# Performance work log

Measured on AMD Instinct MI355X. Metric: run time of the kernel, lower is better.

Reference implementation:

```python
import jax, jax.numpy as jnp
import numpy as np

DIM = 512
N_HEADS = 8
HEAD_DIM = DIM // N_HEADS
TOP_K_RATIO = 0.25
B, L = 2, 2048


def setup_inputs() -> dict:
    key = jax.random.key(0)
    k1, k2, k3, k4, k5 = jax.random.split(key, 5)
    s = 0.02
    return {
        "x": jax.random.normal(k1, (B, L, DIM), jnp.float32),
        "w_qkv": jax.random.normal(k2, (3 * DIM, DIM), jnp.float32) * s,
        "b_qkv": jnp.zeros((3 * DIM,), jnp.float32),
        "w_out": jax.random.normal(k3, (DIM, DIM), jnp.float32) * s,
        "b_out": jnp.zeros((DIM,), jnp.float32),
    }


def reference(x, w_qkv, b_qkv, w_out, b_out):
    Bx, Lx, C = x.shape
    scale = HEAD_DIM ** -0.5
    top_k = max(1, int(TOP_K_RATIO * Lx))

    qkv = x @ w_qkv.T + b_qkv  # [B, L, 3*C]
    qkv = qkv.reshape(Bx, Lx, 3, N_HEADS, HEAD_DIM)
    q, k, v = qkv[:, :, 0], qkv[:, :, 1], qkv[:, :, 2]  # [B, L, H, D]

    scores = jnp.einsum('blhd,bshd->bhls', q, k) * scale  # [B, H, L, L]

    _, top_idx = jax.lax.top_k(scores, top_k)  # [B, H, L, K]
    bi = jnp.arange(Bx)[:, None, None, None]
    hi = jnp.arange(N_HEADS)[None, :, None, None]
    li = jnp.arange(Lx)[None, None, :, None]
    mask = jnp.zeros(scores.shape, bool).at[bi, hi, li, top_idx].set(True)

    masked = jnp.where(mask, scores, -jnp.inf)
    probs = jax.nn.softmax(masked, axis=-1)  # [B, H, L, L]

    out = jnp.einsum('bhls,bshd->blhd', probs, v).reshape(Bx, Lx, C)
    return out @ w_out.T + b_out
```

## Files before the change

kernel.cpp:

```cpp
#include <hip/hip_runtime.h>

#define B_ 2
#define L_ 2048
#define DIM_ 512
#define NH_ 8
#define HD_ 64
#define TOPK_ 512

typedef __attribute__((ext_vector_type(8))) short short8;
typedef __attribute__((ext_vector_type(4))) float f32x4;
typedef unsigned short ushort_t;

__device__ __forceinline__ unsigned f2ord(float f) {
  unsigned u = __float_as_uint(f);
  return (u >> 31) ? ~u : (u | 0x80000000u);
}
__device__ __forceinline__ float ord2f(unsigned k) {
  unsigned u = (k >> 31) ? (k ^ 0x80000000u) : ~k;
  return __uint_as_float(u);
}
__device__ __forceinline__ ushort_t bfrne(float f) {
  unsigned u = __float_as_uint(f);
  return (ushort_t)((u + 0x7FFFu + ((u >> 16) & 1u)) >> 16);
}

__global__ __launch_bounds__(256) void split_k(
    const float* __restrict__ src, ushort_t* __restrict__ dh,
    ushort_t* __restrict__ dl, int n8)
{
  const int i = blockIdx.x * 256 + threadIdx.x;
  if (i >= n8) return;
  const float4 a = ((const float4*)src)[2 * i];
  const float4 b = ((const float4*)src)[2 * i + 1];
  float f[8] = {a.x, a.y, a.z, a.w, b.x, b.y, b.z, b.w};
  short8 h, l;
#pragma unroll
  for (int j = 0; j < 8; ++j) {
    const ushort_t hi = bfrne(f[j]);
    const float hf = __uint_as_float((unsigned)hi << 16);
    h[j] = (short)hi;
    l[j] = (short)bfrne(f[j] - hf);
  }
  *(short8*)(dh + 8 * (size_t)i) = h;
  *(short8*)(dl + 8 * (size_t)i) = l;
}

template<int EPI>
__global__ __launch_bounds__(128, 2) void mgemm(
    const ushort_t* __restrict__ Ah, const ushort_t* __restrict__ Al,
    const ushort_t* __restrict__ Bh, const ushort_t* __restrict__ Bl,
    const float* __restrict__ bias, int N, float* __restrict__ out,
    ushort_t* __restrict__ Qh, ushort_t* __restrict__ Ql,
    ushort_t* __restrict__ Kh, ushort_t* __restrict__ Kl,
    ushort_t* __restrict__ Vt)
{
  constexpr int K = DIM_;
  const int lane = threadIdx.x & 63, wid = threadIdx.x >> 6;
  const int m0 = blockIdx.y * 64;
  const int n0 = blockIdx.x * 64 + wid * 32;
  const int arow = lane & 15, agrp = lane >> 4;

  f32x4 acc[4][2];
#pragma unroll
  for (int rt = 0; rt < 4; ++rt)
#pragma unroll
    for (int ct = 0; ct < 2; ++ct) acc[rt][ct] = (f32x4){0.f, 0.f, 0.f, 0.f};

#pragma unroll 4
  for (int ks = 0; ks < K / 32; ++ks) {
    const int ko = ks * 32 + agrp * 8;
    short8 ah[4], al[4];
#pragma unroll
    for (int rt = 0; rt < 4; ++rt) {
      const size_t ao = (size_t)(m0 + rt * 16 + arow) * K + ko;
      ah[rt] = *(const short8*)(Ah + ao);
      al[rt] = *(const short8*)(Al + ao);
    }
    short8 bhf[2], blf[2];
#pragma unroll
    for (int ct = 0; ct < 2; ++ct) {
      const size_t bo = (size_t)(n0 + ct * 16 + arow) * K + ko;
      bhf[ct] = *(const short8*)(Bh + bo);
      blf[ct] = *(const short8*)(Bl + bo);
    }
#pragma unroll
    for (int rt = 0; rt < 4; ++rt)
#pragma unroll
      for (int ct = 0; ct < 2; ++ct) {
        acc[rt][ct] = __builtin_amdgcn_mfma_f32_16x16x32_bf16(ah[rt], bhf[ct], acc[rt][ct], 0, 0, 0);
        acc[rt][ct] = __builtin_amdgcn_mfma_f32_16x16x32_bf16(al[rt], bhf[ct], acc[rt][ct], 0, 0, 0);
        acc[rt][ct] = __builtin_amdgcn_mfma_f32_16x16x32_bf16(ah[rt], blf[ct], acc[rt][ct], 0, 0, 0);
      }
  }

#pragma unroll
  for (int rt = 0; rt < 4; ++rt) {
#pragma unroll
    for (int ct = 0; ct < 2; ++ct) {
#pragma unroll
      for (int rr = 0; rr < 4; ++rr) {
        const int m = m0 + rt * 16 + agrp * 4 + rr;
        const int n = n0 + ct * 16 + arow;
        float v = acc[rt][ct][rr] + bias[n];
        if (EPI == 0) {
          out[(size_t)m * N + n] = v;
        } else {
          const int b = m >> 11, l = m & (L_ - 1);
          const int which = n >> 9, h = (n >> 6) & (NH_ - 1), d = n & (HD_ - 1);
          const int bh = b * NH_ + h;
          if (which == 0) {
            v *= 0.125f;
            ushort_t hi = bfrne(v);
            float hf = __uint_as_float((unsigned)hi << 16);
            ushort_t lo = bfrne(v - hf);
            const size_t o = ((size_t)bh * L_ + l) * HD_ + d;
            Qh[o] = hi; Ql[o] = lo;
          } else if (which == 1) {
            ushort_t hi = bfrne(v);
            float hf = __uint_as_float((unsigned)hi << 16);
            ushort_t lo = bfrne(v - hf);
            const size_t o = ((size_t)bh * L_ + l) * HD_ + d;
            Kh[o] = hi; Kl[o] = lo;
          } else {
            Vt[((size_t)bh * HD_ + d) * L_ + l] = bfrne(v);
          }
        }
      }
    }
  }
}

__global__ __launch_bounds__(256, 4) void sgemm_k(
    const ushort_t* __restrict__ Qh, const ushort_t* __restrict__ Ql,
    const ushort_t* __restrict__ Kh, const ushort_t* __restrict__ Kl,
    float* __restrict__ S, int row0, int CH)
{
  const int lane = threadIdx.x & 63, wid = threadIdx.x >> 6;
  const int bh = blockIdx.z;
  const int m0 = blockIdx.y * 64;
  const int n0 = blockIdx.x * 128 + wid * 32;
  const int arow = lane & 15, agrp = lane >> 4;

  short8 kh[2][2], kl[2][2];
#pragma unroll
  for (int kt = 0; kt < 2; ++kt) {
    const size_t ka = ((size_t)bh * L_ + n0 + kt * 16 + arow) * HD_ + agrp * 8;
    kh[kt][0] = *(const short8*)(Kh + ka);
    kh[kt][1] = *(const short8*)(Kh + ka + 32);
    kl[kt][0] = *(const short8*)(Kl + ka);
    kl[kt][1] = *(const short8*)(Kl + ka + 32);
  }

  float* schunk = S + (size_t)bh * CH * L_;
#pragma unroll
  for (int rt = 0; rt < 4; ++rt) {
    const size_t qa = ((size_t)bh * L_ + row0 + m0 + rt * 16 + arow) * HD_ + agrp * 8;
    const short8 qh0 = *(const short8*)(Qh + qa);
    const short8 qh1 = *(const short8*)(Qh + qa + 32);
    const short8 ql0 = *(const short8*)(Ql + qa);
    const short8 ql1 = *(const short8*)(Ql + qa + 32);
#pragma unroll
    for (int kt = 0; kt < 2; ++kt) {
      f32x4 aA = {0.f, 0.f, 0.f, 0.f}, aB = {0.f, 0.f, 0.f, 0.f};
      aA = __builtin_amdgcn_mfma_f32_16x16x32_bf16(qh0, kh[kt][0], aA, 0, 0, 0);
      aB = __builtin_amdgcn_mfma_f32_16x16x32_bf16(qh1, kh[kt][1], aB, 0, 0, 0);
      aA = __builtin_amdgcn_mfma_f32_16x16x32_bf16(ql0, kh[kt][0], aA, 0, 0, 0);
      aB = __builtin_amdgcn_mfma_f32_16x16x32_bf16(ql1, kh[kt][1], aB, 0, 0, 0);
      aA = __builtin_amdgcn_mfma_f32_16x16x32_bf16(qh0, kl[kt][0], aA, 0, 0, 0);
      aB = __builtin_amdgcn_mfma_f32_16x16x32_bf16(qh1, kl[kt][1], aB, 0, 0, 0);
#pragma unroll
      for (int rr = 0; rr < 4; ++rr)
        schunk[(size_t)(m0 + rt * 16 + agrp * 4 + rr) * L_ + n0 + kt * 16 + arow]
            = aA[rr] + aB[rr];
    }
  }
}

__global__ __launch_bounds__(512, 8) void selpv_k(
    const float* __restrict__ S, const ushort_t* __restrict__ Vt,
    ushort_t* __restrict__ AOh, ushort_t* __restrict__ AOl, int row0, int CH)
{
  __shared__ ushort_t pl[8][2056];
  __shared__ float invs[8];
  float* red = (float*)&pl[0][0];

  const int tid = threadIdx.x, lane = tid & 63, wid = tid >> 6;
  const int bh = blockIdx.y;
  const int blk = blockIdx.x;
  const int arow = lane & 15, agrp = lane >> 4;

  {
    const float* srow = S + ((size_t)bh * CH + blk * 8 + wid) * L_;
    unsigned keys[32];
    float mx = -3.0e38f;
#pragma unroll
    for (int t = 0; t < 32; ++t) {
      const float s = srow[lane + 64 * t];
      keys[t] = f2ord(s);
      mx = fmaxf(mx, s);
    }
#pragma unroll
    for (int off = 32; off; off >>= 1) mx = fmaxf(mx, __shfl_xor(mx, off));

    unsigned P = 0;
#pragma unroll 1
    for (int bit = 31; bit >= 8; --bit) {
      const unsigned cand = P | (1u << bit);
      int c = 0;
#pragma unroll
      for (int t = 0; t < 32; ++t)
        c += (int)__popcll(__ballot(keys[t] >= cand));
      if (c >= TOPK_) P = cand;
    }

    int base = 0;
    float part = 0.f;
#pragma unroll
    for (int t = 0; t < 32; ++t) {
      const bool sel = keys[t] >= P;
      const unsigned long long mb = __ballot(sel);
      const int pos = base + (int)__popcll(mb & ((1ull << lane) - 1ull));
      const float p = (sel && pos < TOPK_) ? __expf(ord2f(keys[t]) - mx) : 0.f;
      pl[wid][lane + 64 * t] = bfrne(p);
      part += p;
      base += (int)__popcll(mb);
    }
#pragma unroll
    for (int off = 32; off; off >>= 1) part += __shfl_xor(part, off);
    if (lane == 0) invs[wid] = 1.f / part;
  }
  __syncthreads();

  f32x4 o0 = {0.f,0.f,0.f,0.f}, o1 = o0, o2 = o0, o3 = o0;
  {
    const int key00 = wid << 8;
    const size_t vrow = ((size_t)bh * HD_ + arow) * L_;
#pragma unroll 2
    for (int ks = 0; ks < 8; ++ks) {
      const int kb = key00 + ks * 32 + agrp * 8;
      const short8 pa = *(const short8*)&pl[arow & 7][kb];
      const size_t vb0 = vrow + kb;
      const short8 v0 = *(const short8*)(Vt + vb0);
      const short8 v1 = *(const short8*)(Vt + vb0 + 16 * L_);
      const short8 v2 = *(const short8*)(Vt + vb0 + 32 * L_);
      const short8 v3 = *(const short8*)(Vt + vb0 + 48 * L_);
      o0 = __builtin_amdgcn_mfma_f32_16x16x32_bf16(pa, v0, o0, 0, 0, 0);
      o1 = __builtin_amdgcn_mfma_f32_16x16x32_bf16(pa, v1, o1, 0, 0, 0);
      o2 = __builtin_amdgcn_mfma_f32_16x16x32_bf16(pa, v2, o2, 0, 0, 0);
      o3 = __builtin_amdgcn_mfma_f32_16x16x32_bf16(pa, v3, o3, 0, 0, 0);
    }
  }
  __syncthreads();

  if (agrp < 2) {
#pragma unroll
    for (int rr = 0; rr < 4; ++rr) {
      const int row = agrp * 4 + rr;
      red[wid * 512 + row * 64 +  0 + arow] = o0[rr];
      red[wid * 512 + row * 64 + 16 + arow] = o1[rr];
      red[wid * 512 + row * 64 + 32 + arow] = o2[rr];
      red[wid * 512 + row * 64 + 48 + arow] = o3[rr];
    }
  }
  __syncthreads();
  {
    const int b = bh >> 3, h = bh & 7;
    const int r = tid >> 6, d = tid & 63;
    float s = 0.f;
#pragma unroll
    for (int w = 0; w < 8; ++w) s += red[w * 512 + r * 64 + d];
    const float sv = s * invs[r];
    const ushort_t hi = bfrne(sv);
    const float hf = __uint_as_float((unsigned)hi << 16);
    const size_t oidx = ((size_t)(b * L_ + row0 + blk * 8 + r)) * DIM_ + h * HD_ + d;
    AOh[oidx] = hi;
    AOl[oidx] = bfrne(sv - hf);
  }
}

__global__ __launch_bounds__(1024, 1) void attn_fused_k(
    const ushort_t* __restrict__ Qh, const ushort_t* __restrict__ Ql,
    const ushort_t* __restrict__ Kh, const ushort_t* __restrict__ Kl,
    const ushort_t* __restrict__ Vt,
    ushort_t* __restrict__ AOh, ushort_t* __restrict__ AOl)
{
  __shared__ float sc[16][2052];
  __shared__ float invs[16];

  const int tid = threadIdx.x, lane = tid & 63, wid = tid >> 6;
  const int bh = blockIdx.x >> 7;
  const int l0 = (blockIdx.x & 127) << 4;
  const int arow = lane & 15, agrp = lane >> 4;
  const int key00 = wid << 7;

  const size_t qbase = ((size_t)bh * L_ + l0 + arow) * HD_ + agrp * 8;
  const short8 qh0 = *(const short8*)(Qh + qbase);
  const short8 qh1 = *(const short8*)(Qh + qbase + 32);
  const short8 ql0 = *(const short8*)(Ql + qbase);
  const short8 ql1 = *(const short8*)(Ql + qbase + 32);

  {
#pragma unroll
    for (int t = 0; t < 8; ++t) {
      const int key0 = key00 + t * 16;
      const size_t ka = ((size_t)bh * L_ + key0 + arow) * HD_ + agrp * 8;
      const short8 kh0 = *(const short8*)(Kh + ka);
      const short8 kh1 = *(const short8*)(Kh + ka + 32);
      const short8 kl0 = *(const short8*)(Kl + ka);
      const short8 kl1 = *(const short8*)(Kl + ka + 32);
      f32x4 aA = {0.f, 0.f, 0.f, 0.f}, aB = {0.f, 0.f, 0.f, 0.f};
      aA = __builtin_amdgcn_mfma_f32_16x16x32_bf16(qh0, kh0, aA, 0, 0, 0);
      aB = __builtin_amdgcn_mfma_f32_16x16x32_bf16(qh1, kh1, aB, 0, 0, 0);
      aA = __builtin_amdgcn_mfma_f32_16x16x32_bf16(ql0, kh0, aA, 0, 0, 0);
      aB = __builtin_amdgcn_mfma_f32_16x16x32_bf16(ql1, kh1, aB, 0, 0, 0);
      aA = __builtin_amdgcn_mfma_f32_16x16x32_bf16(qh0, kl0, aA, 0, 0, 0);
      aB = __builtin_amdgcn_mfma_f32_16x16x32_bf16(qh1, kl1, aB, 0, 0, 0);
#pragma unroll
      for (int rr = 0; rr < 4; ++rr)
        sc[agrp * 4 + rr][key0 + arow] = aA[rr] + aB[rr];
    }
  }
  __syncthreads();

  {
    const int r = wid;
    unsigned keys[32];
    float mx = -3.0e38f;
#pragma unroll
    for (int t = 0; t < 32; ++t) {
      const float s = sc[r][lane + 64 * t];
      keys[t] = f2ord(s);
      mx = fmaxf(mx, s);
    }
#pragma unroll
    for (int off = 32; off; off >>= 1) mx = fmaxf(mx, __shfl_xor(mx, off));

    unsigned P = 0;
#pragma unroll 1
    for (int bit = 31; bit >= 8; --bit) {
      const unsigned cand = P | (1u << bit);
      int c = 0;
#pragma unroll
      for (int t = 0; t < 32; ++t)
        c += (int)__popcll(__ballot(keys[t] >= cand));
      if (c >= TOPK_) P = cand;
    }

    int base = 0;
    float part = 0.f;
#pragma unroll
    for (int t = 0; t < 32; ++t) {
      const bool sel = keys[t] >= P;
      const unsigned long long mb = __ballot(sel);
      const int pos = base + (int)__popcll(mb & ((1ull << lane) - 1ull));
      const float p = (sel && pos < TOPK_) ? __expf(ord2f(keys[t]) - mx) : 0.f;
      sc[r][lane + 64 * t] = p;
      part += p;
      base += (int)__popcll(mb);
    }
#pragma unroll
    for (int off = 32; off; off >>= 1) part += __shfl_xor(part, off);
    if (lane == 0) invs[r] = 1.f / part;
  }
  __syncthreads();

  f32x4 o0 = {0.f,0.f,0.f,0.f}, o1 = o0, o2 = o0, o3 = o0;
  {
    const size_t vrow = ((size_t)bh * HD_ + arow) * L_;
#pragma unroll
    for (int ks = 0; ks < 4; ++ks) {
      const int kb = key00 + ks * 32 + agrp * 8;
      float pf[8];
      *(float4*)&pf[0] = *(const float4*)&sc[arow][kb];
      *(float4*)&pf[4] = *(const float4*)&sc[arow][kb + 4];
      short8 pa;
#pragma unroll
      for (int j = 0; j < 8; ++j) pa[j] = (short)bfrne(pf[j]);
      const size_t vb0 = vrow + kb;
      const short8 v0 = *(const short8*)(Vt + vb0);
      const short8 v1 = *(const short8*)(Vt + vb0 + 16 * L_);
      const short8 v2 = *(const short8*)(Vt + vb0 + 32 * L_);
      const short8 v3 = *(const short8*)(Vt + vb0 + 48 * L_);
      o0 = __builtin_amdgcn_mfma_f32_16x16x32_bf16(pa, v0, o0, 0, 0, 0);
      o1 = __builtin_amdgcn_mfma_f32_16x16x32_bf16(pa, v1, o1, 0, 0, 0);
      o2 = __builtin_amdgcn_mfma_f32_16x16x32_bf16(pa, v2, o2, 0, 0, 0);
      o3 = __builtin_amdgcn_mfma_f32_16x16x32_bf16(pa, v3, o3, 0, 0, 0);
    }
  }
  __syncthreads();

  float* red = &sc[0][0];
  {
#pragma unroll
    for (int rr = 0; rr < 4; ++rr) {
      const int row = agrp * 4 + rr;
      red[wid * 1024 + row * 64 +  0 + arow] = o0[rr];
      red[wid * 1024 + row * 64 + 16 + arow] = o1[rr];
      red[wid * 1024 + row * 64 + 32 + arow] = o2[rr];
      red[wid * 1024 + row * 64 + 48 + arow] = o3[rr];
    }
  }
  __syncthreads();
  {
    const int b = bh >> 3, h = bh & 7;
    const int r = tid >> 6, d = tid & 63;
    float s = 0.f;
#pragma unroll
    for (int w = 0; w < 16; ++w) s += red[w * 1024 + tid];
    const float sv = s * invs[r];
    const ushort_t hi = bfrne(sv);
    const float hf = __uint_as_float((unsigned)hi << 16);
    const size_t oidx = ((size_t)(b * L_ + l0 + r)) * DIM_ + h * HD_ + d;
    AOh[oidx] = hi;
    AOl[oidx] = bfrne(sv - hf);
  }
}

extern "C" void kernel_launch(void* const* d_in, const int* in_sizes, int n_in,
                              void* d_out, int out_size, void* d_ws, size_t ws_size,
                              hipStream_t stream) {
  const float* x     = (const float*)d_in[0];
  const float* w_qkv = (const float*)d_in[1];
  const float* b_qkv = (const float*)d_in[2];
  const float* w_out = (const float*)d_in[3];
  const float* b_out = (const float*)d_in[4];
  float* out = (float*)d_out;

  const size_t NE  = (size_t)B_ * NH_ * L_ * HD_;
  const size_t NWQ = (size_t)3 * DIM_ * DIM_;
  const size_t NWO = (size_t)DIM_ * DIM_;

  ushort_t* us  = (ushort_t*)d_ws;
  ushort_t* Qh  = us;
  ushort_t* Ql  = Qh + NE;
  ushort_t* Kh  = Ql + NE;
  ushort_t* Kl  = Kh + NE;
  ushort_t* Vt  = Kl + NE;
  ushort_t* AOh = Vt + NE;
  ushort_t* AOl = AOh + NE;
  ushort_t* woh = AOl + NE;
  ushort_t* wol = woh + NWO;
  ushort_t* xh  = wol + NWO;
  ushort_t* xl  = xh + NE;
  ushort_t* wqh = xl + NE;
  ushort_t* wql = wqh + NWQ;
  float*    S   = (float*)xh;

  const size_t sOffB   = (size_t)(7 * NE + 2 * NWO) * sizeof(ushort_t);
  const size_t perRowB = (size_t)B_ * NH_ * L_ * sizeof(float);

  int CH = 0;
  const int cands[6] = {1024, 512, 2048, 256, 128, 64};
  for (int i = 0; i < 6; ++i)
    if (sOffB + (size_t)cands[i] * perRowB <= ws_size) { CH = cands[i]; break; }

  split_k<<<(int)((NE  / 8 + 255) / 256), 256, 0, stream>>>(x,     xh,  xl,  (int)(NE  / 8));
  split_k<<<(int)((NWQ / 8 + 255) / 256), 256, 0, stream>>>(w_qkv, wqh, wql, (int)(NWQ / 8));
  split_k<<<(int)((NWO / 8 + 255) / 256), 256, 0, stream>>>(w_out, woh, wol, (int)(NWO / 8));

  mgemm<1><<<dim3((3 * DIM_) / 64, (B_ * L_) / 64), 128, 0, stream>>>(
      xh, xl, wqh, wql, b_qkv, 3 * DIM_, nullptr, Qh, Ql, Kh, Kl, Vt);

  if (CH) {
    for (int row0 = 0; row0 < L_; row0 += CH) {
      sgemm_k<<<dim3(L_ / 128, CH / 64, B_ * NH_), 256, 0, stream>>>(
          Qh, Ql, Kh, Kl, S, row0, CH);
      selpv_k<<<dim3(CH / 8, B_ * NH_), 512, 0, stream>>>(S, Vt, AOh, AOl, row0, CH);
    }
  } else {
    attn_fused_k<<<dim3(B_ * NH_ * (L_ / 16)), 1024, 0, stream>>>(
        Qh, Ql, Kh, Kl, Vt, AOh, AOl);
  }

  mgemm<0><<<dim3(DIM_ / 64, (B_ * L_) / 64), 128, 0, stream>>>(
      AOh, AOl, woh, wol, b_out, DIM_, out, nullptr, nullptr, nullptr, nullptr, nullptr);
}
```

Baseline: 385.8 us.

## Merge score GEMM and select-PV into one kernel with double-buffered chunks

Replaces the separate score-GEMM and top-k/PV kernels with a single kernel whose blocks are split by index between computing scores for chunk i+1 and doing selection plus PV for chunk i. Two score buffers of 512 rows are used in ping-pong order across five launches, so the memory-heavy GEMM writes overlap the compute-heavy selection within one launch. The GEMM path now runs with 512 threads covering 256 columns per block. The cost is a larger workspace requirement and mixed block types, which can leave resources unbalanced.

```diff
diff --git a/kernel.cpp b/kernel.cpp
--- a/kernel.cpp
+++ b/kernel.cpp
@@ -6,6 +6,7 @@
 #define NH_ 8
 #define HD_ 64
 #define TOPK_ 512
+#define SCH_ 512
 
 typedef __attribute__((ext_vector_type(8))) short short8;
 typedef __attribute__((ext_vector_type(4))) float f32x4;
@@ -130,67 +131,71 @@
   }
 }
 
-__global__ __launch_bounds__(256, 4) void sgemm_k(
+__global__ __launch_bounds__(512, 4) void fat_k(
     const ushort_t* __restrict__ Qh, const ushort_t* __restrict__ Ql,
     const ushort_t* __restrict__ Kh, const ushort_t* __restrict__ Kl,
-    float* __restrict__ S, int row0, int CH)
-{
-  const int lane = threadIdx.x & 63, wid = threadIdx.x >> 6;
-  const int bh = blockIdx.z;
-  const int m0 = blockIdx.y * 64;
-  const int n0 = blockIdx.x * 128 + wid * 32;
-  const int arow = lane & 15, agrp = lane >> 4;
-
-  short8 kh[2][2], kl[2][2];
-#pragma unroll
-  for (int kt = 0; kt < 2; ++kt) {
-    const size_t ka = ((size_t)bh * L_ + n0 + kt * 16 + arow) * HD_ + agrp * 8;
-    kh[kt][0] = *(const short8*)(Kh + ka);
-    kh[kt][1] = *(const short8*)(Kh + ka + 32);
-    kl[kt][0] = *(const short8*)(Kl + ka);
-    kl[kt][1] = *(const short8*)(Kl + ka + 32);
-  }
-
-  float* schunk = S + (size_t)bh * CH * L_;
-#pragma unroll
-  for (int rt = 0; rt < 4; ++rt) {
-    const size_t qa = ((size_t)bh * L_ + row0 + m0 + rt * 16 + arow) * HD_ + agrp * 8;
-    const short8 qh0 = *(const short8*)(Qh + qa);
-    const short8 qh1 = *(const short8*)(Qh + qa + 32);
-    const short8 ql0 = *(const short8*)(Ql + qa);
-    const short8 ql1 = *(const short8*)(Ql + qa + 32);
-#pragma unroll
-    for (int kt = 0; kt < 2; ++kt) {
-      f32x4 aA = {0.f, 0.f, 0.f, 0.f}, aB = {0.f, 0.f, 0.f, 0.f};
-      aA = __builtin_amdgcn_mfma_f32_16x16x32_bf16(qh0, kh[kt][0], aA, 0, 0, 0);
-      aB = __builtin_amdgcn_mfma_f32_16x16x32_bf16(qh1, kh[kt][1], aB, 0, 0, 0);
-      aA = __builtin_amdgcn_mfma_f32_16x16x32_bf16(ql0, kh[kt][0], aA, 0, 0, 0);
-      aB = __builtin_amdgcn_mfma_f32_16x16x32_bf16(ql1, kh[kt][1], aB, 0, 0, 0);
-      aA = __builtin_amdgcn_mfma_f32_16x16x32_bf16(qh0, kl[kt][0], aA, 0, 0, 0);
-      aB = __builtin_amdgcn_mfma_f32_16x16x32_bf16(qh1, kl[kt][1], aB, 0, 0, 0);
-#pragma unroll
-      for (int rr = 0; rr < 4; ++rr)
-        schunk[(size_t)(m0 + rt * 16 + agrp * 4 + rr) * L_ + n0 + kt * 16 + arow]
-            = aA[rr] + aB[rr];
-    }
-  }
-}
-
-__global__ __launch_bounds__(512, 8) void selpv_k(
-    const float* __restrict__ S, const ushort_t* __restrict__ Vt,
-    ushort_t* __restrict__ AOh, ushort_t* __restrict__ AOl, int row0, int CH)
+    const ushort_t* __restrict__ Vt,
+    float* __restrict__ Ssg, int sgRow0, int nsg,
+    const float* __restrict__ Ssp, int spRow0, int nsp,
+    ushort_t* __restrict__ AOh, ushort_t* __restrict__ AOl)
 {
   __shared__ ushort_t pl[8][2056];
   __shared__ float invs[8];
   float* red = (float*)&pl[0][0];
 
   const int tid = threadIdx.x, lane = tid & 63, wid = tid >> 6;
-  const int bh = blockIdx.y;
-  const int blk = blockIdx.x;
   const int arow = lane & 15, agrp = lane >> 4;
 
-  {
-    const float* srow = S + ((size_t)bh * CH + blk * 8 + wid) * L_;
+  int sub; bool isSg;
+  if (nsg && nsp) { isSg = !(blockIdx.x & 1); sub = blockIdx.x >> 1; }
+  else            { isSg = (nsg != 0);        sub = blockIdx.x; }
+
+  if (isSg) {
+    const int bh = sub >> 6, rem = sub & 63;
+    const int m0 = (rem >> 3) * 64;
+    const int n0 = (rem & 7) * 256 + wid * 32;
+
+    short8 kh[2][2], kl[2][2];
+#pragma unroll
+    for (int kt = 0; kt < 2; ++kt) {
+      const size_t ka = ((size_t)bh * L_ + n0 + kt * 16 + arow) * HD_ + agrp * 8;
+      kh[kt][0] = *(const short8*)(Kh + ka);
+      kh[kt][1] = *(const short8*)(Kh + ka + 32);
+      kl[kt][0] = *(const short8*)(Kl + ka);
+      kl[kt][1] = *(const short8*)(Kl + ka + 32);
+    }
+
+    float* schunk = Ssg + (size_t)bh * SCH_ * L_;
+#pragma unroll
+    for (int rt = 0; rt < 4; ++rt) {
+      const size_t qa = ((size_t)bh * L_ + sgRow0 + m0 + rt * 16 + arow) * HD_ + agrp * 8;
+      const short8 qh0 = *(const short8*)(Qh + qa);
+      const short8 qh1 = *(const short8*)(Qh + qa + 32);
+      const short8 ql0 = *(const short8*)(Ql + qa);
+      const short8 ql1 = *(const short8*)(Ql + qa + 32);
+#pragma unroll
+      for (int kt = 0; kt < 2; ++kt) {
+        f32x4 aA = {0.f, 0.f, 0.f, 0.f}, aB = {0.f, 0.f, 0.f, 0.f};
+        aA = __builtin_amdgcn_mfma_f32_16x16x32_bf16(qh0, kh[kt][0], aA, 0, 0, 0);
+        aB = __builtin_amdgcn_mfma_f32_16x16x32_bf16(qh1, kh[kt][1], aB, 0, 0, 0);
+        aA = __builtin_amdgcn_mfma_f32_16x16x32_bf16(ql0, kh[kt][0], aA, 0, 0, 0);
+        aB = __builtin_amdgcn_mfma_f32_16x16x32_bf16(ql1, kh[kt][1], aB, 0, 0, 0);
+        aA = __builtin_amdgcn_mfma_f32_16x16x32_bf16(qh0, kl[kt][0], aA, 0, 0, 0);
+        aB = __builtin_amdgcn_mfma_f32_16x16x32_bf16(qh1, kl[kt][1], aB, 0, 0, 0);
+#pragma unroll
+        for (int rr = 0; rr < 4; ++rr)
+          schunk[(size_t)(m0 + rt * 16 + agrp * 4 + rr) * L_ + n0 + kt * 16 + arow]
+              = aA[rr] + aB[rr];
+      }
+    }
+    return;
+  }
+
+  const int bh = sub >> 6;
+  const int blk = sub & 63;
+
+  {
+    const float* srow = Ssp + ((size_t)bh * SCH_ + blk * 8 + wid) * L_;
     unsigned keys[32];
     float mx = -3.0e38f;
 #pragma unroll
@@ -272,7 +277,7 @@
     const float sv = s * invs[r];
     const ushort_t hi = bfrne(sv);
     const float hf = __uint_as_float((unsigned)hi << 16);
-    const size_t oidx = ((size_t)(b * L_ + row0 + blk * 8 + r)) * DIM_ + h * HD_ + d;
+    const size_t oidx = ((size_t)(b * L_ + spRow0 + blk * 8 + r)) * DIM_ + h * HD_ + d;
     AOh[oidx] = hi;
     AOl[oidx] = bfrne(sv - hf);
   }
@@ -444,15 +449,13 @@
   ushort_t* xl  = xh + NE;
   ushort_t* wqh = xl + NE;
   ushort_t* wql = wqh + NWQ;
-  float*    S   = (float*)xh;
-
-  const size_t sOffB   = (size_t)(7 * NE + 2 * NWO) * sizeof(ushort_t);
-  const size_t perRowB = (size_t)B_ * NH_ * L_ * sizeof(float);
-
-  int CH = 0;
-  const int cands[6] = {1024, 512, 2048, 256, 128, 64};
-  for (int i = 0; i < 6; ++i)
-    if (sOffB + (size_t)cands[i] * perRowB <= ws_size) { CH = cands[i]; break; }
+
+  const size_t SCHN = (size_t)B_ * NH_ * SCH_ * L_;
+  float* S0 = (float*)xh;
+  float* S1 = S0 + SCHN;
+
+  const size_t sOffB = (size_t)(7 * NE + 2 * NWO) * sizeof(ushort_t);
+  const size_t need  = sOffB + 2 * SCHN * sizeof(float);
 
   split_k<<<(int)((NE  / 8 + 255) / 256), 256, 0, stream>>>(x,     xh,  xl,  (int)(NE  / 8));
   split_k<<<(int)((NWQ / 8 + 255) / 256), 256, 0, stream>>>(w_qkv, wqh, wql, (int)(NWQ / 8));
@@ -461,12 +464,17 @@
   mgemm<1><<<dim3((3 * DIM_) / 64, (B_ * L_) / 64), 128, 0, stream>>>(
       xh, xl, wqh, wql, b_qkv, 3 * DIM_, nullptr, Qh, Ql, Kh, Kl, Vt);
 
-  if (CH) {
-    for (int row0 = 0; row0 < L_; row0 += CH) {
-      sgemm_k<<<dim3(L_ / 128, CH / 64, B_ * NH_), 256, 0, stream>>>(
-          Qh, Ql, Kh, Kl, S, row0, CH);
-      selpv_k<<<dim3(CH / 8, B_ * NH_), 512, 0, stream>>>(S, Vt, AOh, AOl, row0, CH);
-    }
+  if (ws_size >= need) {
+    fat_k<<<1024, 512, 0, stream>>>(Qh, Ql, Kh, Kl, Vt,
+        S0, 0, 1024, S1, 0, 0, AOh, AOl);
+    fat_k<<<2048, 512, 0, stream>>>(Qh, Ql, Kh, Kl, Vt,
+        S1, 512, 1024, S0, 0, 1024, AOh, AOl);
+    fat_k<<<2048, 512, 0, stream>>>(Qh, Ql, Kh, Kl, Vt,
+        S0, 1024, 1024, S1, 512, 1024, AOh, AOl);
+    fat_k<<<2048, 512, 0, stream>>>(Qh, Ql, Kh, Kl, Vt,
+        S1, 1536, 1024, S0, 1024, 1024, AOh, AOl);
+    fat_k<<<1024, 512, 0, stream>>>(Qh, Ql, Kh, Kl, Vt,
+        S0, 0, 0, S1, 1536, 1024, AOh, AOl);
   } else {
     attn_fused_k<<<dim3(B_ * NH_ * (L_ / 16)), 1024, 0, stream>>>(
         Qh, Ql, Kh, Kl, Vt, AOh, AOl);
```

New measurement: 536.2 us. 39.0% more time.
